# Optimization experiments

Hardware: AMD Instinct MI355X
Metric: run time of the kernel (lower is better)

## Reference

```python
import jax, jax.numpy as jnp
import numpy as np


def setup_inputs() -> dict:
    key = jax.random.key(0)
    k1, k2 = jax.random.split(key)
    shape = (16, 64, 32, 28, 28)  # (b, c, t, h, w)
    x = jax.random.normal(k1, shape, dtype=jnp.float32)
    x_v = jax.random.normal(k2, shape, dtype=jnp.float32)
    return {"x": x, "x_v": x_v}


def reference(x, x_v):
    b, c, t, h, w = x.shape
    d = c * h * w
    # (b, t, d): flatten channel+spatial into feature dim per frame
    r_q = jnp.transpose(x, (0, 2, 1, 3, 4)).reshape(b, t, d)
    r_v = jnp.transpose(x_v, (0, 2, 1, 3, 4)).reshape(b, t, d)
    # (b, t, t) frame-frame similarity
    m_t = jnp.einsum('bqd,bkd->bqk', r_q, r_q)
    # NOTE: softmax over the BATCH axis (dim=0), faithful to the original
    m_t = jax.nn.softmax(m_t, axis=0)
    a_t = jnp.einsum('bqk,bkd->bqd', m_t, r_v)
    a = a_t.reshape(b, t, c, h, w).transpose(0, 2, 1, 3, 4)
    return a
```

## Files before the change

### kernel.cpp

```cpp
#include <hip/hip_runtime.h>

namespace {

constexpr int Tt = 32;
constexpr int Ss = 784;

using bf16x8 = __attribute__((ext_vector_type(8))) short;
using f32x4  = __attribute__((ext_vector_type(4))) float;

__device__ inline void cvt2(float a, float b, unsigned& h, unsigned& l) {
  const unsigned ha = __float_as_uint(a) >> 16;
  const unsigned hb = __float_as_uint(b) >> 16;
  const float ra = a - __uint_as_float(ha << 16);
  const float rb = b - __uint_as_float(hb << 16);
  const unsigned la = __float_as_uint(ra) >> 16;
  const unsigned lb = __float_as_uint(rb) >> 16;
  h = ha | (hb << 16);
  l = la | (lb << 16);
}

__device__ inline void gload16(const float* g, float* l) {
  __builtin_amdgcn_global_load_lds(
      (const __attribute__((address_space(1))) void*)g,
      (__attribute__((address_space(3))) void*)l, 16, 0, 0);
}

__global__ __launch_bounds__(256, 4) void gram_partial(const float* __restrict__ x,
                                                       float* __restrict__ part) {
  const int bc = blockIdx.x;
  const float* __restrict__ xb = x + (size_t)bc * (Tt * Ss);
  const int tid  = threadIdx.x;
  const int w    = tid >> 6;
  const int lane = tid & 63;
  const int col  = lane & 15;
  const int g    = lane >> 4;

  f32x4 d1[2][2], d2[2][2], d3[2][2];
#pragma unroll
  for (int i = 0; i < 2; ++i)
#pragma unroll
    for (int j = 0; j < 2; ++j) { d1[i][j] = 0.f; d2[i][j] = 0.f; d3[i][j] = 0.f; }

  const float* __restrict__ pa = xb + (size_t)col * Ss;
  const float* __restrict__ pb = xb + (size_t)(16 + col) * Ss;

  for (int ks = w; ks < 25; ks += 4) {
    const int s0 = ks * 32 + g * 8;
    uint4 ha = {0u,0u,0u,0u}, la = {0u,0u,0u,0u};
    uint4 hb = {0u,0u,0u,0u}, lb = {0u,0u,0u,0u};
    if (s0 < 784) {
      const float4 a0 = *reinterpret_cast<const float4*>(pa + s0);
      const float4 a1 = *reinterpret_cast<const float4*>(pa + s0 + 4);
      const float4 b0 = *reinterpret_cast<const float4*>(pb + s0);
      const float4 b1 = *reinterpret_cast<const float4*>(pb + s0 + 4);
      cvt2(a0.x, a0.y, ha.x, la.x);
      cvt2(a0.z, a0.w, ha.y, la.y);
      cvt2(a1.x, a1.y, ha.z, la.z);
      cvt2(a1.z, a1.w, ha.w, la.w);
      cvt2(b0.x, b0.y, hb.x, lb.x);
      cvt2(b0.z, b0.w, hb.y, lb.y);
      cvt2(b1.x, b1.y, hb.z, lb.z);
      cvt2(b1.z, b1.w, hb.w, lb.w);
    }
    const bf16x8 h0 = __builtin_bit_cast(bf16x8, ha);
    const bf16x8 l0 = __builtin_bit_cast(bf16x8, la);
    const bf16x8 h1 = __builtin_bit_cast(bf16x8, hb);
    const bf16x8 l1 = __builtin_bit_cast(bf16x8, lb);
    d1[0][0] = __builtin_amdgcn_mfma_f32_16x16x32_bf16(h0, h0, d1[0][0], 0, 0, 0);
    d1[0][1] = __builtin_amdgcn_mfma_f32_16x16x32_bf16(h0, h1, d1[0][1], 0, 0, 0);
    d1[1][0] = __builtin_amdgcn_mfma_f32_16x16x32_bf16(h1, h0, d1[1][0], 0, 0, 0);
    d1[1][1] = __builtin_amdgcn_mfma_f32_16x16x32_bf16(h1, h1, d1[1][1], 0, 0, 0);
    d2[0][0] = __builtin_amdgcn_mfma_f32_16x16x32_bf16(h0, l0, d2[0][0], 0, 0, 0);
    d2[0][1] = __builtin_amdgcn_mfma_f32_16x16x32_bf16(h0, l1, d2[0][1], 0, 0, 0);
    d2[1][0] = __builtin_amdgcn_mfma_f32_16x16x32_bf16(h1, l0, d2[1][0], 0, 0, 0);
    d2[1][1] = __builtin_amdgcn_mfma_f32_16x16x32_bf16(h1, l1, d2[1][1], 0, 0, 0);
    d3[0][0] = __builtin_amdgcn_mfma_f32_16x16x32_bf16(l0, h0, d3[0][0], 0, 0, 0);
    d3[0][1] = __builtin_amdgcn_mfma_f32_16x16x32_bf16(l0, h1, d3[0][1], 0, 0, 0);
    d3[1][0] = __builtin_amdgcn_mfma_f32_16x16x32_bf16(l1, h0, d3[1][0], 0, 0, 0);
    d3[1][1] = __builtin_amdgcn_mfma_f32_16x16x32_bf16(l1, h1, d3[1][1], 0, 0, 0);
  }

  __shared__ float mtmp[4 * 1056];
#pragma unroll
  for (int i = 0; i < 2; ++i)
#pragma unroll
    for (int j = 0; j < 2; ++j) {
      const f32x4 s4 = d1[i][j] + d2[i][j] + d3[i][j];
#pragma unroll
      for (int r = 0; r < 4; ++r) {
        const int row = i * 16 + g * 4 + r;
        const int cc  = j * 16 + col;
        mtmp[w * 1056 + row * 33 + cc] = s4[r];
      }
    }
  __syncthreads();

  const int e0 = tid * 4;
  float tmp[4];
#pragma unroll
  for (int u = 0; u < 4; ++u) {
    const int row = (e0 + u) >> 5;
    const int cc  = (e0 + u) & 31;
    float ss = 0.f;
#pragma unroll
    for (int ww = 0; ww < 4; ++ww) ss += mtmp[ww * 1056 + row * 33 + cc];
    tmp[u] = ss;
  }
  float4 o4;
  o4.x = tmp[0]; o4.y = tmp[1]; o4.z = tmp[2]; o4.w = tmp[3];
  *reinterpret_cast<float4*>(part + (size_t)bc * 1024 + e0) = o4;
}

__global__ __launch_bounds__(256) void reduce_c(const float* __restrict__ part,
                                                float* __restrict__ msum) {
  const int bid = blockIdx.x;
  const int b   = bid >> 2;
  const int e   = (bid & 3) * 256 + threadIdx.x;
  const float* __restrict__ p = part + (size_t)b * 64 * 1024 + e;
  float s0 = 0.f, s1 = 0.f, s2 = 0.f, s3 = 0.f;
#pragma unroll
  for (int c = 0; c < 64; c += 4) {
    s0 += p[(size_t)(c + 0) * 1024];
    s1 += p[(size_t)(c + 1) * 1024];
    s2 += p[(size_t)(c + 2) * 1024];
    s3 += p[(size_t)(c + 3) * 1024];
  }
  msum[b * 1024 + e] = (s0 + s1) + (s2 + s3);
}

__global__ __launch_bounds__(256) void softmax_b(const float* __restrict__ msum,
                                                 float* __restrict__ mq) {
  const int e = blockIdx.x * 256 + threadIdx.x;
  float l[16];
  float mx = -3.4e38f;
#pragma unroll
  for (int b = 0; b < 16; ++b) {
    l[b] = msum[b * 1024 + e];
    mx = fmaxf(mx, l[b]);
  }
  float s = 0.f;
#pragma unroll
  for (int b = 0; b < 16; ++b) {
    l[b] = expf(l[b] - mx);
    s += l[b];
  }
  const float inv = 1.f / s;
#pragma unroll
  for (int b = 0; b < 16; ++b) mq[b * 1024 + e] = l[b] * inv;
}

__global__ __launch_bounds__(256, 4) void pv(const float* __restrict__ xv,
                                             const float* __restrict__ mq,
                                             float* __restrict__ out) {
  const int gbl = blockIdx.x;
  const int bc  = gbl >> 2;
  const int ch  = gbl & 3;
  const int b   = bc >> 6;
  const int off = ch * 192;
  const float* __restrict__ xvb = xv + (size_t)bc * (Tt * Ss);
  float* __restrict__ ob        = out + (size_t)bc * (Tt * Ss);

  const int tid  = threadIdx.x;
  const int w    = tid >> 6;
  const int lane = tid & 63;
  const int col  = lane & 15;
  const int g    = lane >> 4;

  __shared__ float lds[32 * 208];

  bf16x8 mh[2], ml[2];
#pragma unroll
  for (int qf = 0; qf < 2; ++qf) {
    const float* mp = mq + b * 1024 + (qf * 16 + col) * 32 + g * 8;
    const float4 ma = *reinterpret_cast<const float4*>(mp);
    const float4 mb = *reinterpret_cast<const float4*>(mp + 4);
    uint4 h, l;
    cvt2(ma.x, ma.y, h.x, l.x);
    cvt2(ma.z, ma.w, h.y, l.y);
    cvt2(mb.x, mb.y, h.z, l.z);
    cvt2(mb.z, mb.w, h.w, l.w);
    mh[qf] = __builtin_bit_cast(bf16x8, h);
    ml[qf] = __builtin_bit_cast(bf16x8, l);
  }

#pragma unroll
  for (int round = 0; round < 6; ++round) {
    const int v   = round * 256 + tid;
    const int row = v / 52;
    const int c4  = v - row * 52;
    gload16(xvb + row * Ss + off + c4 * 4,
            &lds[(round * 256 + w * 64) * 4]);
  }
  if (tid < 128) {
    const int v   = 1536 + tid;
    const int row = v / 52;
    const int c4  = v - row * 52;
    gload16(xvb + row * Ss + off + c4 * 4, &lds[(1536 + w * 64) * 4]);
  }
  __syncthreads();

  const int nfrag = (ch == 3) ? 13 : 12;
  const int fend  = (w == 3) ? nfrag : 3 * w + 3;
  for (int sf = 3 * w; sf < fend; ++sf) {
    float f8[8];
#pragma unroll
    for (int j = 0; j < 8; ++j)
      f8[j] = lds[(8 * g + j) * 208 + sf * 16 + col];
    uint4 hh, lv;
    cvt2(f8[0], f8[1], hh.x, lv.x);
    cvt2(f8[2], f8[3], hh.y, lv.y);
    cvt2(f8[4], f8[5], hh.z, lv.z);
    cvt2(f8[6], f8[7], hh.w, lv.w);
    const bf16x8 vh = __builtin_bit_cast(bf16x8, hh);
    const bf16x8 vl = __builtin_bit_cast(bf16x8, lv);
    const int s0 = off + sf * 16;
#pragma unroll
    for (int qf = 0; qf < 2; ++qf) {
      f32x4 d = {0.f, 0.f, 0.f, 0.f};
      d = __builtin_amdgcn_mfma_f32_16x16x32_bf16(vl, mh[qf], d, 0, 0, 0);
      d = __builtin_amdgcn_mfma_f32_16x16x32_bf16(vh, ml[qf], d, 0, 0, 0);
      d = __builtin_amdgcn_mfma_f32_16x16x32_bf16(vh, mh[qf], d, 0, 0, 0);
      float4 o4;
      o4.x = d[0]; o4.y = d[1]; o4.z = d[2]; o4.w = d[3];
      *reinterpret_cast<float4*>(ob + (size_t)(qf * 16 + col) * Ss + s0 + 4 * g) = o4;
    }
  }
}

}

extern "C" void kernel_launch(void* const* d_in, const int* in_sizes, int n_in,
                              void* d_out, int out_size, void* d_ws, size_t ws_size,
                              hipStream_t stream) {
  const float* x  = (const float*)d_in[0];
  const float* xv = (const float*)d_in[1];
  float* out = (float*)d_out;

  float* part = (float*)d_ws;
  float* msum = part + 1024 * 1024;
  float* mq   = msum + 16 * 1024;

  gram_partial<<<dim3(1024), dim3(256), 0, stream>>>(x, part);
  reduce_c<<<dim3(64), dim3(256), 0, stream>>>(part, msum);
  softmax_b<<<dim3(4), dim3(256), 0, stream>>>(msum, mq);
  pv<<<dim3(4096), dim3(256), 0, stream>>>(xv, mq, out);
}
```

Before: 76.91 us.

## Double-buffer xv chunks in pv kernel with one block per (b,c) slice

```diff
diff --git a/kernel.cpp b/kernel.cpp
--- a/kernel.cpp
+++ b/kernel.cpp
@@ -152,11 +152,8 @@
 __global__ __launch_bounds__(256, 4) void pv(const float* __restrict__ xv,
                                              const float* __restrict__ mq,
                                              float* __restrict__ out) {
-  const int gbl = blockIdx.x;
-  const int bc  = gbl >> 2;
-  const int ch  = gbl & 3;
-  const int b   = bc >> 6;
-  const int off = ch * 192;
+  const int bc = blockIdx.x;
+  const int b  = bc >> 6;
   const float* __restrict__ xvb = xv + (size_t)bc * (Tt * Ss);
   float* __restrict__ ob        = out + (size_t)bc * (Tt * Ss);
 
@@ -166,7 +163,7 @@
   const int col  = lane & 15;
   const int g    = lane >> 4;
 
-  __shared__ float lds[32 * 208];
+  __shared__ float lds[2][32 * 128];
 
   bf16x8 mh[2], ml[2];
 #pragma unroll
@@ -183,29 +180,70 @@
     ml[qf] = __builtin_bit_cast(bf16x8, l);
   }
 
-#pragma unroll
-  for (int round = 0; round < 6; ++round) {
-    const int v   = round * 256 + tid;
-    const int row = v / 52;
-    const int c4  = v - row * 52;
-    gload16(xvb + row * Ss + off + c4 * 4,
-            &lds[(round * 256 + w * 64) * 4]);
-  }
-  if (tid < 128) {
-    const int v   = 1536 + tid;
-    const int row = v / 52;
-    const int c4  = v - row * 52;
-    gload16(xvb + row * Ss + off + c4 * 4, &lds[(1536 + w * 64) * 4]);
-  }
-  __syncthreads();
-
-  const int nfrag = (ch == 3) ? 13 : 12;
-  const int fend  = (w == 3) ? nfrag : 3 * w + 3;
-  for (int sf = 3 * w; sf < fend; ++sf) {
+  auto stage = [&](int buf, int ch) {
+    const int off = ch * 128;
+#pragma unroll
+    for (int round = 0; round < 4; ++round) {
+      const int v   = round * 256 + tid;
+      const int row = v >> 5;
+      const int c4  = v & 31;
+      gload16(xvb + row * Ss + off + c4 * 4,
+              &lds[buf][(round * 256 + w * 64) * 4]);
+    }
+  };
+
+  stage(0, 0);
+  stage(1, 1);
+
+#pragma unroll
+  for (int ch = 0; ch < 6; ++ch) {
+    if (ch == 0 || ch == 5) {
+      asm volatile("s_waitcnt vmcnt(4)" ::: "memory");
+    } else {
+      asm volatile("s_waitcnt vmcnt(8)" ::: "memory");
+    }
+    __builtin_amdgcn_sched_barrier(0);
+    __builtin_amdgcn_s_barrier();
+
+    const float* __restrict__ lbuf = lds[ch & 1];
+    const int off = ch * 128;
+#pragma unroll
+    for (int fi = 0; fi < 2; ++fi) {
+      const int sf = 2 * w + fi;
+      float f8[8];
+#pragma unroll
+      for (int j = 0; j < 8; ++j)
+        f8[j] = lbuf[(8 * g + j) * 128 + sf * 16 + col];
+      uint4 hh, lv;
+      cvt2(f8[0], f8[1], hh.x, lv.x);
+      cvt2(f8[2], f8[3], hh.y, lv.y);
+      cvt2(f8[4], f8[5], hh.z, lv.z);
+      cvt2(f8[6], f8[7], hh.w, lv.w);
+      const bf16x8 vh = __builtin_bit_cast(bf16x8, hh);
+      const bf16x8 vl = __builtin_bit_cast(bf16x8, lv);
+      const int s0 = off + sf * 16;
+#pragma unroll
+      for (int qf = 0; qf < 2; ++qf) {
+        f32x4 d = {0.f, 0.f, 0.f, 0.f};
+        d = __builtin_amdgcn_mfma_f32_16x16x32_bf16(vl, mh[qf], d, 0, 0, 0);
+        d = __builtin_amdgcn_mfma_f32_16x16x32_bf16(vh, ml[qf], d, 0, 0, 0);
+        d = __builtin_amdgcn_mfma_f32_16x16x32_bf16(vh, mh[qf], d, 0, 0, 0);
+        float4 o4;
+        o4.x = d[0]; o4.y = d[1]; o4.z = d[2]; o4.w = d[3];
+        *reinterpret_cast<float4*>(ob + (size_t)(qf * 16 + col) * Ss + s0 + 4 * g) = o4;
+      }
+    }
+    asm volatile("s_waitcnt lgkmcnt(0)" ::: "memory");
+    __builtin_amdgcn_sched_barrier(0);
+    __builtin_amdgcn_s_barrier();
+    if (ch < 4) stage(ch & 1, ch + 2);
+  }
+
+  if (w == 3) {
     float f8[8];
 #pragma unroll
     for (int j = 0; j < 8; ++j)
-      f8[j] = lds[(8 * g + j) * 208 + sf * 16 + col];
+      f8[j] = xvb[(size_t)(8 * g + j) * Ss + 768 + col];
     uint4 hh, lv;
     cvt2(f8[0], f8[1], hh.x, lv.x);
     cvt2(f8[2], f8[3], hh.y, lv.y);
@@ -213,7 +251,6 @@
     cvt2(f8[6], f8[7], hh.w, lv.w);
     const bf16x8 vh = __builtin_bit_cast(bf16x8, hh);
     const bf16x8 vl = __builtin_bit_cast(bf16x8, lv);
-    const int s0 = off + sf * 16;
 #pragma unroll
     for (int qf = 0; qf < 2; ++qf) {
       f32x4 d = {0.f, 0.f, 0.f, 0.f};
@@ -222,7 +259,7 @@
       d = __builtin_amdgcn_mfma_f32_16x16x32_bf16(vh, mh[qf], d, 0, 0, 0);
       float4 o4;
       o4.x = d[0]; o4.y = d[1]; o4.z = d[2]; o4.w = d[3];
-      *reinterpret_cast<float4*>(ob + (size_t)(qf * 16 + col) * Ss + s0 + 4 * g) = o4;
+      *reinterpret_cast<float4*>(ob + (size_t)(qf * 16 + col) * Ss + 768 + 4 * g) = o4;
     }
   }
 }
@@ -243,5 +280,5 @@
   gram_partial<<<dim3(1024), dim3(256), 0, stream>>>(x, part);
   reduce_c<<<dim3(64), dim3(256), 0, stream>>>(part, msum);
   softmax_b<<<dim3(4), dim3(256), 0, stream>>>(msum, mq);
-  pv<<<dim3(4096), dim3(256), 0, stream>>>(xv, mq, out);
-}
+  pv<<<dim3(1024), dim3(256), 0, stream>>>(xv, mq, out);
+}
```

New measurement: 73.43 us (median of 2 runs). 1.05x faster.
